# Optimization experiments

Measured on AMD Instinct MI355X. Metric: run time of the kernel, lower is better.

The kernel has to match this reference:

```python
import jax, jax.numpy as jnp
import numpy as np

N, H, E, C, V, K = 4096, 256, 128, 32, 64, 20


def setup_inputs() -> dict:
    key = jax.random.key(0)
    ks = jax.random.split(key, 16)
    f = lambda k, s: jax.random.normal(k, s, dtype=jnp.float32)
    return {
        "vec": f(ks[0], (N, H)),
        "inp": f(ks[1], (N, E)),
        "h_prev": f(ks[2], (N, H)),
        "c_prev": f(ks[3], (N, H)),
        "Wlin": f(ks[4], (C, V, H)) * 0.05,
        "blin": f(ks[5], (C, V)) * 0.05,
        "Wec": f(ks[6], (2, H)) * 0.05,
        "bec": f(ks[7], (2,)) * 0.05,
        "Wrel": f(ks[8], (5, H)) * 0.05,
        "brel": f(ks[9], (5,)) * 0.05,
        "W_ih": f(ks[10], (K, 4 * H, E)) * 0.05,
        "b_ih": f(ks[11], (K, 4 * H)) * 0.05,
        "W_hh": f(ks[12], (K, 4 * H, H)) * 0.05,
        "b_hh": f(ks[13], (K, 4 * H)) * 0.05,
        "category": jax.random.randint(ks[14], (N,), 0, C, dtype=jnp.int32),
        "cell_id": jax.random.randint(ks[15], (N,), 0, K, dtype=jnp.int32),
        "true_idx": jax.random.randint(jax.random.fold_in(key, 100), (N,), 0, V, dtype=jnp.int32),
        "ec_idx": jax.random.randint(jax.random.fold_in(key, 101), (N,), 0, 2, dtype=jnp.int32),
        "rel_idx": jax.random.randint(jax.random.fold_in(key, 102), (N,), 0, 5, dtype=jnp.int32),
    }


def _ce(logits, targets):
    # per-row cross entropy (same math as nn.CrossEntropyLoss per example)
    logp = jax.nn.log_softmax(logits, axis=-1)
    return -jnp.take_along_axis(logp, targets[:, None], axis=-1)[:, 0]


def reference(vec, inp, h_prev, c_prev, Wlin, blin, Wec, bec, Wrel, brel,
              W_ih, b_ih, W_hh, b_hh, category, cell_id, true_idx, ec_idx, rel_idx):
    # --- get_log_odds: per-category tiny linear head, selected by category ---
    logits_all = jnp.einsum('nh,cvh->ncv', vec, Wlin) + blin          # [N,C,V]
    logits = jnp.take_along_axis(logits_all, category[:, None, None].astype(jnp.int32), axis=1)[:, 0]  # [N,V]
    logits_ec = vec @ Wec.T + bec                                      # [N,2]
    logits_rel = vec @ Wrel.T + brel                                   # [N,5]

    # --- calculate_loss: CE over valid children + ec + rel ---
    losses = _ce(logits, true_idx) + _ce(logits_ec, ec_idx) + _ce(logits_rel, rel_idx)  # [N]

    # --- get_next: per-child-index LSTMCell, selected by cell_id ---
    gates_all = (jnp.einsum('ne,kge->nkg', inp, W_ih)
                 + jnp.einsum('nh,kgh->nkg', h_prev, W_hh)
                 + b_ih + b_hh)                                        # [N,K,4H]
    gates = jnp.take_along_axis(gates_all, cell_id[:, None, None].astype(jnp.int32), axis=1)[:, 0]  # [N,4H]
    i, f, g, o = jnp.split(gates, 4, axis=-1)                          # torch LSTMCell gate order i,f,g,o
    c_next = jax.nn.sigmoid(f) * c_prev + jax.nn.sigmoid(i) * jnp.tanh(g)
    h_next = jax.nn.sigmoid(o) * jnp.tanh(c_next)

    # pack: [N, 1 + 2H] = loss | h_next | c_next
    return jnp.concatenate([losses[:, None], h_next, c_next], axis=-1)
```

## Files before the change

kernel.cpp:

```cpp
#include <hip/hip_runtime.h>
#include <hip/hip_bf16.h>
#include <math.h>

#define Nn 4096
#define Hdim 256
#define Edim 128
#define Cdim 32
#define Vdim 64
#define Kdim 20
#define G4H 1024
#define OUTS 513

#define NB 8
#define LMAXL 96
#define MAXG (NB * LMAXL)
#define MAXT2 192
#define GRID (MAXG + MAXT2)

typedef short bf16x8 __attribute__((ext_vector_type(8)));
typedef float f32x4 __attribute__((ext_vector_type(4)));

__device__ __forceinline__ float sigmoidf_(float x) { return 1.0f / (1.0f + expf(-x)); }

__device__ __forceinline__ bf16x8 cvt8(float4 f0, float4 f1) {
    bf16x8 r;
    __hip_bfloat16 h;
    h = __float2bfloat16(f0.x); r[0] = *(short*)&h;
    h = __float2bfloat16(f0.y); r[1] = *(short*)&h;
    h = __float2bfloat16(f0.z); r[2] = *(short*)&h;
    h = __float2bfloat16(f0.w); r[3] = *(short*)&h;
    h = __float2bfloat16(f1.x); r[4] = *(short*)&h;
    h = __float2bfloat16(f1.y); r[5] = *(short*)&h;
    h = __float2bfloat16(f1.z); r[6] = *(short*)&h;
    h = __float2bfloat16(f1.w); r[7] = *(short*)&h;
    return r;
}

__device__ __forceinline__ void gl_lds16(const float* g, void* l) {
    __builtin_amdgcn_global_load_lds((const __attribute__((address_space(1))) void*)g,
                                     (__attribute__((address_space(3))) void*)l, 16, 0, 0);
}

__device__ __forceinline__ int swz(int r) { return ((r & 3) << 1) | ((r >> 2) & 1); }

__global__ __launch_bounds__(256, 4) void k_all(
    const float* __restrict__ vec, const float* __restrict__ inp,
    const float* __restrict__ h_prev, const float* __restrict__ c_prev,
    const float* __restrict__ Wlin, const float* __restrict__ blin,
    const float* __restrict__ Wec, const float* __restrict__ bec,
    const float* __restrict__ Wrel, const float* __restrict__ brel,
    const float* __restrict__ W_ih, const float* __restrict__ b_ih,
    const float* __restrict__ W_hh, const float* __restrict__ b_hh,
    const int* __restrict__ category, const int* __restrict__ cell_id,
    const int* __restrict__ true_idx, const int* __restrict__ ec_idx, const int* __restrict__ rel_idx,
    float* __restrict__ out)
{
    __shared__ __align__(16) char smem[40960];
    int* cntR = (int*)smem;
    int* cntF = (int*)(smem + 8192);
    int* wsum = (int*)(smem + 8320);
    int* rows_tmp = (int*)(smem + 8448);

    int t = threadIdx.x;
    int w = t >> 6, l = t & 63;
    int l15 = l & 15, quad = l >> 4;
    int lrow8 = l >> 3, lslot = l & 7;
    bool is_lstm = blockIdx.x < MAXG;
    const int* key = is_lstm ? cell_id : category;
    int nbins = is_lstm ? Kdim : Cdim;

    for (int i = t; i < nbins * 16; i += 256) cntR[i] = 0;
    __syncthreads();
    int4 kv0 = ((const int4*)key)[t * 4 + 0];
    int4 kv1 = ((const int4*)key)[t * 4 + 1];
    int4 kv2 = ((const int4*)key)[t * 4 + 2];
    int4 kv3 = ((const int4*)key)[t * 4 + 3];
    int ks[16] = { kv0.x, kv0.y, kv0.z, kv0.w, kv1.x, kv1.y, kv1.z, kv1.w,
                   kv2.x, kv2.y, kv2.z, kv2.w, kv3.x, kv3.y, kv3.z, kv3.w };
    int rep = t & 15;
    #pragma unroll
    for (int j = 0; j < 16; j++) atomicAdd(&cntR[ks[j] * 16 + rep], 1);
    __syncthreads();
    if (t < nbins) {
        int s2 = 0;
        #pragma unroll
        for (int r2 = 0; r2 < 16; r2++) s2 += cntR[t * 16 + r2];
        cntF[t] = s2;
    }
    __syncthreads();

    int myk, s_idx, hb0 = 0, rcount, wlen;
    if (is_lstm) {
        int b = blockIdx.x & 7, pos = blockIdx.x >> 3;
        int u = -1, sf = 0, acc = 0;
        for (int uu = b; uu < Kdim * 4; uu += NB) {
            int n = (cntF[uu >> 2] + 63) >> 6;
            if (u < 0 && pos < acc + n) { u = uu; sf = pos - acc; }
            acc += n;
        }
        if (u < 0) return;
        myk = u >> 2; hb0 = (u & 3) * 64; s_idx = sf;
        wlen = 64;
        rcount = min(64, cntF[myk] - s_idx * 64);
    } else {
        int slot = blockIdx.x - MAXG;
        int u = -1, sf = 0, acc = 0;
        for (int m = 0; m < Cdim; m++) {
            int n = (cntF[m] + 31) >> 5;
            if (u < 0 && slot < acc + n) { u = m; sf = slot - acc; }
            acc += n;
        }
        if (u < 0) return;
        myk = u; s_idx = sf;
        wlen = 32;
        rcount = min(32, cntF[myk] - s_idx * 32);
    }

    {
        int local = 0;
        #pragma unroll
        for (int j = 0; j < 16; j++) local += (ks[j] == myk) ? 1 : 0;
        int v = local;
        #pragma unroll
        for (int off = 1; off < 64; off <<= 1) {
            int n = __shfl_up(v, off);
            if (l >= off) v += n;
        }
        if (l == 63) wsum[w] = v;
        __syncthreads();
        int wbase = 0;
        #pragma unroll
        for (int ww = 0; ww < 4; ww++) wbase += (ww < w) ? wsum[ww] : 0;
        int rank = wbase + v - local;
        int w0 = s_idx * wlen;
        #pragma unroll
        for (int j = 0; j < 16; j++) {
            if (ks[j] == myk) {
                int rr = rank - w0;
                if (rr >= 0 && rr < wlen) rows_tmp[rr] = t * 16 + j;
                rank++;
            }
        }
        __syncthreads();
        if (t < wlen && t >= rcount) rows_tmp[t] = rows_tmp[0];
        __syncthreads();
    }
    int reg_row = rows_tmp[is_lstm ? l : (l & 31)];
    int swz_l = swz(l15);
    int p0 = (quad * 2) ^ swz_l;

    if (is_lstm) {
        float* Wbuf = (float*)smem;
        float* Xbuf = (float*)(smem + 32768);
        const float* Wih_k = W_ih + (size_t)myk * G4H * Edim;
        const float* Whh_k = W_hh + (size_t)myk * G4H * Hdim;

        int xr0 = w * 16 + lrow8;
        int xr1 = w * 16 + 8 + lrow8;
        int xrow0 = __shfl(reg_row, xr0);
        int xrow1 = __shfl(reg_row, xr1);
        int xg0 = lslot ^ swz(xr0);
        int xg1 = lslot ^ swz(xr1);

        f32x4 acc[4][4];
        #pragma unroll
        for (int m = 0; m < 4; m++)
            #pragma unroll
            for (int g = 0; g < 4; g++)
                acc[m][g] = (f32x4){0.f, 0.f, 0.f, 0.f};

        for (int st = 0; st < 12; st++) {
            int k0 = st * 32;
            const float* Wsrc; int stride, ko;
            if (k0 < Edim) { Wsrc = Wih_k; stride = Edim; ko = k0; }
            else           { Wsrc = Whh_k; stride = Hdim; ko = k0 - Edim; }
            const float* Xs0 = (k0 < Edim) ? inp + (size_t)xrow0 * Edim + ko
                                           : h_prev + (size_t)xrow0 * Hdim + (ko - 0);
            const float* Xs1 = (k0 < Edim) ? inp + (size_t)xrow1 * Edim + ko
                                           : h_prev + (size_t)xrow1 * Hdim + (ko - 0);
            __syncthreads();
            #pragma unroll
            for (int j = 0; j < 8; j++) {
                int r = w * 64 + j * 8 + lrow8;
                int g = lslot ^ swz(r);
                int gate = r >> 6, hl = r & 63;
                gl_lds16(Wsrc + (size_t)(gate * Hdim + hb0 + hl) * stride + ko + g * 4,
                         Wbuf + (w * 64 + j * 8) * 32);
            }
            gl_lds16(Xs0 + xg0 * 4, Xbuf + (w * 16) * 32);
            gl_lds16(Xs1 + xg1 * 4, Xbuf + (w * 16 + 8) * 32);
            __syncthreads();

            bf16x8 af[4], bfr[4];
            #pragma unroll
            for (int m = 0; m < 4; m++) {
                int row = m * 16 + l15;
                float4 lo = *(float4*)(Xbuf + row * 32 + p0 * 4);
                float4 hi = *(float4*)(Xbuf + row * 32 + (p0 ^ 1) * 4);
                af[m] = cvt8(lo, hi);
            }
            #pragma unroll
            for (int g = 0; g < 4; g++) {
                int row = g * 64 + w * 16 + l15;
                float4 lo = *(float4*)(Wbuf + row * 32 + p0 * 4);
                float4 hi = *(float4*)(Wbuf + row * 32 + (p0 ^ 1) * 4);
                bfr[g] = cvt8(lo, hi);
            }
            #pragma unroll
            for (int m = 0; m < 4; m++)
                #pragma unroll
                for (int g = 0; g < 4; g++)
                    acc[m][g] = __builtin_amdgcn_mfma_f32_16x16x32_bf16(af[m], bfr[g], acc[m][g], 0, 0, 0);
        }

        int h = hb0 + w * 16 + l15;
        float bs[4];
        #pragma unroll
        for (int g = 0; g < 4; g++)
            bs[g] = b_ih[(size_t)myk * G4H + g * Hdim + h] + b_hh[(size_t)myk * G4H + g * Hdim + h];

        #pragma unroll
        for (int m = 0; m < 4; m++) {
            #pragma unroll
            for (int reg = 0; reg < 4; reg++) {
                int r = m * 16 + quad * 4 + reg;
                int row = __shfl(reg_row, r);
                if (r < rcount) {
                    float iv = acc[m][0][reg] + bs[0];
                    float fv = acc[m][1][reg] + bs[1];
                    float gv = acc[m][2][reg] + bs[2];
                    float ov = acc[m][3][reg] + bs[3];
                    float cp = c_prev[(size_t)row * Hdim + h];
                    float cn = sigmoidf_(fv) * cp + sigmoidf_(iv) * tanhf(gv);
                    float hn = sigmoidf_(ov) * tanhf(cn);
                    out[(size_t)row * OUTS + 1 + h] = hn;
                    out[(size_t)row * OUTS + 1 + Hdim + h] = cn;
                }
            }
        }
    } else {
        float* Wlbuf = (float*)smem;
        float* Vbuf  = (float*)(smem + 10240);
        float* Lg    = (float*)(smem + 14336);
        int m2 = myk;

        int xr = w * 8 + lrow8;
        int xrow = __shfl(reg_row, xr);
        int xg = lslot ^ swz(xr);

        f32x4 a0[2], a1[2];
        #pragma unroll
        for (int m = 0; m < 2; m++) { a0[m] = (f32x4){0.f,0.f,0.f,0.f}; a1[m] = (f32x4){0.f,0.f,0.f,0.f}; }

        for (int st = 0; st < 8; st++) {
            int ko = st * 32;
            __syncthreads();
            for (int n = w; n < 10; n += 4) {
                int r = n * 8 + lrow8;
                int g = lslot ^ swz(r);
                const float* srcW;
                if (r < 64)      srcW = Wlin + ((size_t)m2 * Vdim + r) * Hdim;
                else if (r < 66) srcW = Wec + (size_t)(r - 64) * Hdim;
                else if (r < 71) srcW = Wrel + (size_t)(r - 66) * Hdim;
                else             srcW = Wlin + (size_t)m2 * Vdim * Hdim;
                gl_lds16(srcW + ko + g * 4, Wlbuf + n * 8 * 32);
            }
            gl_lds16(vec + (size_t)xrow * Hdim + ko + xg * 4, Vbuf + (w * 8) * 32);
            __syncthreads();

            bf16x8 af[2];
            #pragma unroll
            for (int m = 0; m < 2; m++) {
                int row = m * 16 + l15;
                float4 lo = *(float4*)(Vbuf + row * 32 + p0 * 4);
                float4 hi = *(float4*)(Vbuf + row * 32 + (p0 ^ 1) * 4);
                af[m] = cvt8(lo, hi);
            }
            {
                int row = w * 16 + l15;
                float4 lo = *(float4*)(Wlbuf + row * 32 + p0 * 4);
                float4 hi = *(float4*)(Wlbuf + row * 32 + (p0 ^ 1) * 4);
                bf16x8 b0 = cvt8(lo, hi);
                a0[0] = __builtin_amdgcn_mfma_f32_16x16x32_bf16(af[0], b0, a0[0], 0, 0, 0);
                a0[1] = __builtin_amdgcn_mfma_f32_16x16x32_bf16(af[1], b0, a0[1], 0, 0, 0);
            }
            if (w == 3) {
                int row = 64 + l15;
                float4 lo = *(float4*)(Wlbuf + row * 32 + p0 * 4);
                float4 hi = *(float4*)(Wlbuf + row * 32 + (p0 ^ 1) * 4);
                bf16x8 b1 = cvt8(lo, hi);
                a1[0] = __builtin_amdgcn_mfma_f32_16x16x32_bf16(af[0], b1, a1[0], 0, 0, 0);
                a1[1] = __builtin_amdgcn_mfma_f32_16x16x32_bf16(af[1], b1, a1[1], 0, 0, 0);
            }
        }
        __syncthreads();
        {
            int col = w * 16 + l15;
            float bb = blin[m2 * Vdim + col];
            #pragma unroll
            for (int m = 0; m < 2; m++)
                #pragma unroll
                for (int reg = 0; reg < 4; reg++)
                    Lg[(m * 16 + quad * 4 + reg) * 84 + col] = a0[m][reg] + bb;
            if (w == 3) {
                int col1 = 64 + l15;
                float bb1 = (l15 < 2) ? bec[l15] : ((l15 < 7) ? brel[l15 - 2] : 0.f);
                #pragma unroll
                for (int m = 0; m < 2; m++)
                    #pragma unroll
                    for (int reg = 0; reg < 4; reg++)
                        Lg[(m * 16 + quad * 4 + reg) * 84 + col1] = a1[m][reg] + bb1;
            }
        }
        __syncthreads();
        for (int rr = 0; rr < 8; rr++) {
            int r = w * 8 + rr;
            if (r >= rcount) break;
            int orig = __shfl(reg_row, r);
            float lg = Lg[r * 84 + l];
            float mx = lg;
            for (int ss = 32; ss >= 1; ss >>= 1) mx = fmaxf(mx, __shfl_xor(mx, ss));
            float sm = expf(lg - mx);
            for (int ss = 32; ss >= 1; ss >>= 1) sm += __shfl_xor(sm, ss);
            float lt = __shfl(lg, true_idx[orig]);
            float loss = mx + logf(sm) - lt;
            if (l == 0) {
                float l0 = Lg[r * 84 + 64], l1 = Lg[r * 84 + 65];
                float me2 = fmaxf(l0, l1);
                loss += me2 + logf(expf(l0 - me2) + expf(l1 - me2)) - ((ec_idx[orig] == 0) ? l0 : l1);
                float rl[5] = { Lg[r * 84 + 66], Lg[r * 84 + 67], Lg[r * 84 + 68], Lg[r * 84 + 69], Lg[r * 84 + 70] };
                float mr = rl[0];
                #pragma unroll
                for (int i = 1; i < 5; i++) mr = fmaxf(mr, rl[i]);
                float sr = 0.f;
                #pragma unroll
                for (int i = 0; i < 5; i++) sr += expf(rl[i] - mr);
                loss += mr + logf(sr) - rl[rel_idx[orig]];
                out[(size_t)orig * OUTS] = loss;
            }
        }
    }
}

extern "C" void kernel_launch(void* const* d_in, const int* in_sizes, int n_in,
                              void* d_out, int out_size, void* d_ws, size_t ws_size,
                              hipStream_t stream) {
    const float* vec      = (const float*)d_in[0];
    const float* inp      = (const float*)d_in[1];
    const float* h_prev   = (const float*)d_in[2];
    const float* c_prev   = (const float*)d_in[3];
    const float* Wlin     = (const float*)d_in[4];
    const float* blin     = (const float*)d_in[5];
    const float* Wec      = (const float*)d_in[6];
    const float* bec      = (const float*)d_in[7];
    const float* Wrel     = (const float*)d_in[8];
    const float* brel     = (const float*)d_in[9];
    const float* W_ih     = (const float*)d_in[10];
    const float* b_ih     = (const float*)d_in[11];
    const float* W_hh     = (const float*)d_in[12];
    const float* b_hh     = (const float*)d_in[13];
    const int*   category = (const int*)d_in[14];
    const int*   cell_id  = (const int*)d_in[15];
    const int*   true_idx = (const int*)d_in[16];
    const int*   ec_idx   = (const int*)d_in[17];
    const int*   rel_idx  = (const int*)d_in[18];
    float* out = (float*)d_out;

    k_all<<<GRID, 256, 0, stream>>>(
        vec, inp, h_prev, c_prev, Wlin, blin, Wec, bec, Wrel, brel,
        W_ih, b_ih, W_hh, b_hh, category, cell_id, true_idx, ec_idx, rel_idx, out);
}
```

Before: 153.3 us.

## Precompute row bucketing in setup kernel and double-buffer LDS staging

Moves the per-block histogram and rank computation over cell_id/category into a small separate setup kernel that writes per-bucket row lists and counts to workspace, so each main block just reads its row list. The main kernel's K-loops now double-buffer the global-to-LDS loads with explicit vmcnt waits so the next stage's loads overlap the current stage's MFMAs. LDS doubles to 80KB and occupancy drops to 2 blocks, and an extra kernel launch is added. Row order within buckets now depends on atomic order, and buckets are capped at fixed sizes.

After: 144.0 us. 1.06x faster.

```diff
diff --git a/kernel.cpp b/kernel.cpp
--- a/kernel.cpp
+++ b/kernel.cpp
@@ -12,10 +12,15 @@
 #define OUTS 513
 
 #define NB 8
-#define LMAXL 96
+#define LMAXL 64
 #define MAXG (NB * LMAXL)
 #define MAXT2 192
 #define GRID (MAXG + MAXT2)
+
+#define SK 512
+#define SC 256
+#define RK_OFF 64
+#define RC_OFF (RK_OFF + Kdim * SK)
 
 typedef short bf16x8 __attribute__((ext_vector_type(8)));
 typedef float f32x4 __attribute__((ext_vector_type(4)));
@@ -43,7 +48,36 @@
 
 __device__ __forceinline__ int swz(int r) { return ((r & 3) << 1) | ((r >> 2) & 1); }
 
-__global__ __launch_bounds__(256, 4) void k_all(
+__global__ __launch_bounds__(1024) void k_setup(const int* __restrict__ cell_id,
+                                                const int* __restrict__ category,
+                                                int* __restrict__ ws) {
+    __shared__ int cnt[32];
+    int t = threadIdx.x;
+    if (t < 32) cnt[t] = 0;
+    __syncthreads();
+    int i0 = t * 4;
+    if (blockIdx.x == 0) {
+        int4 v = ((const int4*)cell_id)[t];
+        int r;
+        r = atomicAdd(&cnt[v.x], 1); if (r < SK) ws[RK_OFF + v.x * SK + r] = i0 + 0;
+        r = atomicAdd(&cnt[v.y], 1); if (r < SK) ws[RK_OFF + v.y * SK + r] = i0 + 1;
+        r = atomicAdd(&cnt[v.z], 1); if (r < SK) ws[RK_OFF + v.z * SK + r] = i0 + 2;
+        r = atomicAdd(&cnt[v.w], 1); if (r < SK) ws[RK_OFF + v.w * SK + r] = i0 + 3;
+        __syncthreads();
+        if (t < 32) ws[t] = min(cnt[t], SK);
+    } else {
+        int4 v = ((const int4*)category)[t];
+        int r;
+        r = atomicAdd(&cnt[v.x], 1); if (r < SC) ws[RC_OFF + v.x * SC + r] = i0 + 0;
+        r = atomicAdd(&cnt[v.y], 1); if (r < SC) ws[RC_OFF + v.y * SC + r] = i0 + 1;
+        r = atomicAdd(&cnt[v.z], 1); if (r < SC) ws[RC_OFF + v.z * SC + r] = i0 + 2;
+        r = atomicAdd(&cnt[v.w], 1); if (r < SC) ws[RC_OFF + v.w * SC + r] = i0 + 3;
+        __syncthreads();
+        if (t < 32) ws[32 + t] = min(cnt[t], SC);
+    }
+}
+
+__global__ __launch_bounds__(256, 2) void k_main(
     const float* __restrict__ vec, const float* __restrict__ inp,
     const float* __restrict__ h_prev, const float* __restrict__ c_prev,
     const float* __restrict__ Wlin, const float* __restrict__ blin,
@@ -51,159 +85,120 @@
     const float* __restrict__ Wrel, const float* __restrict__ brel,
     const float* __restrict__ W_ih, const float* __restrict__ b_ih,
     const float* __restrict__ W_hh, const float* __restrict__ b_hh,
-    const int* __restrict__ category, const int* __restrict__ cell_id,
     const int* __restrict__ true_idx, const int* __restrict__ ec_idx, const int* __restrict__ rel_idx,
+    const int* __restrict__ ws,
     float* __restrict__ out)
 {
-    __shared__ __align__(16) char smem[40960];
-    int* cntR = (int*)smem;
-    int* cntF = (int*)(smem + 8192);
-    int* wsum = (int*)(smem + 8320);
-    int* rows_tmp = (int*)(smem + 8448);
+    __shared__ __align__(16) char smem[81920];
 
     int t = threadIdx.x;
     int w = t >> 6, l = t & 63;
     int l15 = l & 15, quad = l >> 4;
     int lrow8 = l >> 3, lslot = l & 7;
     bool is_lstm = blockIdx.x < MAXG;
-    const int* key = is_lstm ? cell_id : category;
-    int nbins = is_lstm ? Kdim : Cdim;
-
-    for (int i = t; i < nbins * 16; i += 256) cntR[i] = 0;
+
+    int* cnt = (int*)smem;
+    if (t < 32) cnt[t] = ws[(is_lstm ? 0 : 32) + t];
     __syncthreads();
-    int4 kv0 = ((const int4*)key)[t * 4 + 0];
-    int4 kv1 = ((const int4*)key)[t * 4 + 1];
-    int4 kv2 = ((const int4*)key)[t * 4 + 2];
-    int4 kv3 = ((const int4*)key)[t * 4 + 3];
-    int ks[16] = { kv0.x, kv0.y, kv0.z, kv0.w, kv1.x, kv1.y, kv1.z, kv1.w,
-                   kv2.x, kv2.y, kv2.z, kv2.w, kv3.x, kv3.y, kv3.z, kv3.w };
-    int rep = t & 15;
-    #pragma unroll
-    for (int j = 0; j < 16; j++) atomicAdd(&cntR[ks[j] * 16 + rep], 1);
-    __syncthreads();
-    if (t < nbins) {
-        int s2 = 0;
-        #pragma unroll
-        for (int r2 = 0; r2 < 16; r2++) s2 += cntR[t * 16 + r2];
-        cntF[t] = s2;
-    }
-    __syncthreads();
-
-    int myk, s_idx, hb0 = 0, rcount, wlen;
+
+    int myk, s_idx, hb0 = 0, rcount;
     if (is_lstm) {
         int b = blockIdx.x & 7, pos = blockIdx.x >> 3;
         int u = -1, sf = 0, acc = 0;
         for (int uu = b; uu < Kdim * 4; uu += NB) {
-            int n = (cntF[uu >> 2] + 63) >> 6;
+            int n = (cnt[uu >> 2] + 63) >> 6;
             if (u < 0 && pos < acc + n) { u = uu; sf = pos - acc; }
             acc += n;
         }
         if (u < 0) return;
         myk = u >> 2; hb0 = (u & 3) * 64; s_idx = sf;
-        wlen = 64;
-        rcount = min(64, cntF[myk] - s_idx * 64);
+        rcount = min(64, cnt[myk] - s_idx * 64);
     } else {
         int slot = blockIdx.x - MAXG;
         int u = -1, sf = 0, acc = 0;
         for (int m = 0; m < Cdim; m++) {
-            int n = (cntF[m] + 31) >> 5;
+            int n = (cnt[m] + 31) >> 5;
             if (u < 0 && slot < acc + n) { u = m; sf = slot - acc; }
             acc += n;
         }
         if (u < 0) return;
         myk = u; s_idx = sf;
-        wlen = 32;
-        rcount = min(32, cntF[myk] - s_idx * 32);
+        rcount = min(32, cnt[myk] - s_idx * 32);
     }
 
-    {
-        int local = 0;
-        #pragma unroll
-        for (int j = 0; j < 16; j++) local += (ks[j] == myk) ? 1 : 0;
-        int v = local;
-        #pragma unroll
-        for (int off = 1; off < 64; off <<= 1) {
-            int n = __shfl_up(v, off);
-            if (l >= off) v += n;
-        }
-        if (l == 63) wsum[w] = v;
-        __syncthreads();
-        int wbase = 0;
-        #pragma unroll
-        for (int ww = 0; ww < 4; ww++) wbase += (ww < w) ? wsum[ww] : 0;
-        int rank = wbase + v - local;
-        int w0 = s_idx * wlen;
-        #pragma unroll
-        for (int j = 0; j < 16; j++) {
-            if (ks[j] == myk) {
-                int rr = rank - w0;
-                if (rr >= 0 && rr < wlen) rows_tmp[rr] = t * 16 + j;
-                rank++;
-            }
-        }
-        __syncthreads();
-        if (t < wlen && t >= rcount) rows_tmp[t] = rows_tmp[0];
-        __syncthreads();
-    }
-    int reg_row = rows_tmp[is_lstm ? l : (l & 31)];
+    const int* rlist = is_lstm ? (ws + RK_OFF + myk * SK + s_idx * 64)
+                               : (ws + RC_OFF + myk * SC + s_idx * 32);
+    int li = is_lstm ? l : (l & 31);
+    int reg_row = rlist[li < rcount ? li : rcount - 1];
     int swz_l = swz(l15);
     int p0 = (quad * 2) ^ swz_l;
+    __syncthreads();
 
     if (is_lstm) {
-        float* Wbuf = (float*)smem;
-        float* Xbuf = (float*)(smem + 32768);
         const float* Wih_k = W_ih + (size_t)myk * G4H * Edim;
         const float* Whh_k = W_hh + (size_t)myk * G4H * Hdim;
 
         int xr0 = w * 16 + lrow8;
-        int xr1 = w * 16 + 8 + lrow8;
+        int xr1 = xr0 + 8;
         int xrow0 = __shfl(reg_row, xr0);
         int xrow1 = __shfl(reg_row, xr1);
         int xg0 = lslot ^ swz(xr0);
         int xg1 = lslot ^ swz(xr1);
 
-        f32x4 acc[4][4];
-        #pragma unroll
-        for (int m = 0; m < 4; m++)
-            #pragma unroll
-            for (int g = 0; g < 4; g++)
-                acc[m][g] = (f32x4){0.f, 0.f, 0.f, 0.f};
-
-        for (int st = 0; st < 12; st++) {
+        auto stageL = [&](int st, int d) {
+            float* Wb = (float*)(smem + d * 40960);
+            float* Xb = (float*)(smem + d * 40960 + 32768);
             int k0 = st * 32;
             const float* Wsrc; int stride, ko;
             if (k0 < Edim) { Wsrc = Wih_k; stride = Edim; ko = k0; }
             else           { Wsrc = Whh_k; stride = Hdim; ko = k0 - Edim; }
-            const float* Xs0 = (k0 < Edim) ? inp + (size_t)xrow0 * Edim + ko
-                                           : h_prev + (size_t)xrow0 * Hdim + (ko - 0);
-            const float* Xs1 = (k0 < Edim) ? inp + (size_t)xrow1 * Edim + ko
-                                           : h_prev + (size_t)xrow1 * Hdim + (ko - 0);
-            __syncthreads();
             #pragma unroll
             for (int j = 0; j < 8; j++) {
                 int r = w * 64 + j * 8 + lrow8;
                 int g = lslot ^ swz(r);
                 int gate = r >> 6, hl = r & 63;
                 gl_lds16(Wsrc + (size_t)(gate * Hdim + hb0 + hl) * stride + ko + g * 4,
-                         Wbuf + (w * 64 + j * 8) * 32);
-            }
-            gl_lds16(Xs0 + xg0 * 4, Xbuf + (w * 16) * 32);
-            gl_lds16(Xs1 + xg1 * 4, Xbuf + (w * 16 + 8) * 32);
-            __syncthreads();
-
+                         Wb + (w * 64 + j * 8) * 32);
+            }
+            const float* Xs0 = (k0 < Edim) ? inp + (size_t)xrow0 * Edim + ko
+                                           : h_prev + (size_t)xrow0 * Hdim + ko;
+            const float* Xs1 = (k0 < Edim) ? inp + (size_t)xrow1 * Edim + ko
+                                           : h_prev + (size_t)xrow1 * Hdim + ko;
+            gl_lds16(Xs0 + xg0 * 4, Xb + (w * 16) * 32);
+            gl_lds16(Xs1 + xg1 * 4, Xb + (w * 16 + 8) * 32);
+        };
+
+        f32x4 acc[4][4];
+        #pragma unroll
+        for (int m = 0; m < 4; m++)
+            #pragma unroll
+            for (int g = 0; g < 4; g++)
+                acc[m][g] = (f32x4){0.f, 0.f, 0.f, 0.f};
+
+        stageL(0, 0);
+        for (int st = 0; st < 12; st++) {
+            int cur = st & 1;
+            if (st < 11) stageL(st + 1, cur ^ 1);
+            if (st < 11) asm volatile("s_waitcnt vmcnt(10)" ::: "memory");
+            else         asm volatile("s_waitcnt vmcnt(0)" ::: "memory");
+            __builtin_amdgcn_s_barrier();
+            __builtin_amdgcn_sched_barrier(0);
+
+            float* Wb = (float*)(smem + cur * 40960);
+            float* Xb = (float*)(smem + cur * 40960 + 32768);
             bf16x8 af[4], bfr[4];
             #pragma unroll
             for (int m = 0; m < 4; m++) {
                 int row = m * 16 + l15;
-                float4 lo = *(float4*)(Xbuf + row * 32 + p0 * 4);
-                float4 hi = *(float4*)(Xbuf + row * 32 + (p0 ^ 1) * 4);
+                float4 lo = *(float4*)(Xb + row * 32 + p0 * 4);
+                float4 hi = *(float4*)(Xb + row * 32 + (p0 ^ 1) * 4);
                 af[m] = cvt8(lo, hi);
             }
             #pragma unroll
             for (int g = 0; g < 4; g++) {
                 int row = g * 64 + w * 16 + l15;
-                float4 lo = *(float4*)(Wbuf + row * 32 + p0 * 4);
-                float4 hi = *(float4*)(Wbuf + row * 32 + (p0 ^ 1) * 4);
+                float4 lo = *(float4*)(Wb + row * 32 + p0 * 4);
+                float4 hi = *(float4*)(Wb + row * 32 + (p0 ^ 1) * 4);
                 bfr[g] = cvt8(lo, hi);
             }
             #pragma unroll
@@ -211,6 +206,9 @@
                 #pragma unroll
                 for (int g = 0; g < 4; g++)
                     acc[m][g] = __builtin_amdgcn_mfma_f32_16x16x32_bf16(af[m], bfr[g], acc[m][g], 0, 0, 0);
+
+            __builtin_amdgcn_sched_barrier(0);
+            __builtin_amdgcn_s_barrier();
         }
 
         int h = hb0 + w * 16 + l15;
@@ -239,22 +237,15 @@
             }
         }
     } else {
-        float* Wlbuf = (float*)smem;
-        float* Vbuf  = (float*)(smem + 10240);
-        float* Lg    = (float*)(smem + 14336);
         int m2 = myk;
-
         int xr = w * 8 + lrow8;
         int xrow = __shfl(reg_row, xr);
         int xg = lslot ^ swz(xr);
 
-        f32x4 a0[2], a1[2];
-        #pragma unroll
-        for (int m = 0; m < 2; m++) { a0[m] = (f32x4){0.f,0.f,0.f,0.f}; a1[m] = (f32x4){0.f,0.f,0.f,0.f}; }
-
-        for (int st = 0; st < 8; st++) {
+        auto stageS = [&](int st, int d) {
+            float* Wb = (float*)(smem + d * 14336);
+            float* Vb = (float*)(smem + d * 14336 + 10240);
             int ko = st * 32;
-            __syncthreads();
             for (int n = w; n < 10; n += 4) {
                 int r = n * 8 + lrow8;
                 int g = lslot ^ swz(r);
@@ -263,37 +254,57 @@
                 else if (r < 66) srcW = Wec + (size_t)(r - 64) * Hdim;
                 else if (r < 71) srcW = Wrel + (size_t)(r - 66) * Hdim;
                 else             srcW = Wlin + (size_t)m2 * Vdim * Hdim;
-                gl_lds16(srcW + ko + g * 4, Wlbuf + n * 8 * 32);
-            }
-            gl_lds16(vec + (size_t)xrow * Hdim + ko + xg * 4, Vbuf + (w * 8) * 32);
-            __syncthreads();
-
+                gl_lds16(srcW + ko + g * 4, Wb + n * 8 * 32);
+            }
+            gl_lds16(vec + (size_t)xrow * Hdim + ko + xg * 4, Vb + (w * 8) * 32);
+        };
+
+        f32x4 a0[2], a1[2];
+        #pragma unroll
+        for (int m = 0; m < 2; m++) { a0[m] = (f32x4){0.f,0.f,0.f,0.f}; a1[m] = (f32x4){0.f,0.f,0.f,0.f}; }
+
+        stageS(0, 0);
+        for (int st = 0; st < 8; st++) {
+            int cur = st & 1;
+            if (st < 7) stageS(st + 1, cur ^ 1);
+            if (st < 7) {
+                if (w < 2) asm volatile("s_waitcnt vmcnt(4)" ::: "memory");
+                else       asm volatile("s_waitcnt vmcnt(3)" ::: "memory");
+            } else       asm volatile("s_waitcnt vmcnt(0)" ::: "memory");
+            __builtin_amdgcn_s_barrier();
+            __builtin_amdgcn_sched_barrier(0);
+
+            float* Wb = (float*)(smem + cur * 14336);
+            float* Vb = (float*)(smem + cur * 14336 + 10240);
             bf16x8 af[2];
             #pragma unroll
             for (int m = 0; m < 2; m++) {
                 int row = m * 16 + l15;
-                float4 lo = *(float4*)(Vbuf + row * 32 + p0 * 4);
-                float4 hi = *(float4*)(Vbuf + row * 32 + (p0 ^ 1) * 4);
+                float4 lo = *(float4*)(Vb + row * 32 + p0 * 4);
+                float4 hi = *(float4*)(Vb + row * 32 + (p0 ^ 1) * 4);
                 af[m] = cvt8(lo, hi);
             }
             {
                 int row = w * 16 + l15;
-                float4 lo = *(float4*)(Wlbuf + row * 32 + p0 * 4);
-                float4 hi = *(float4*)(Wlbuf + row * 32 + (p0 ^ 1) * 4);
+                float4 lo = *(float4*)(Wb + row * 32 + p0 * 4);
+                float4 hi = *(float4*)(Wb + row * 32 + (p0 ^ 1) * 4);
                 bf16x8 b0 = cvt8(lo, hi);
                 a0[0] = __builtin_amdgcn_mfma_f32_16x16x32_bf16(af[0], b0, a0[0], 0, 0, 0);
                 a0[1] = __builtin_amdgcn_mfma_f32_16x16x32_bf16(af[1], b0, a0[1], 0, 0, 0);
             }
             if (w == 3) {
                 int row = 64 + l15;
-                float4 lo = *(float4*)(Wlbuf + row * 32 + p0 * 4);
-                float4 hi = *(float4*)(Wlbuf + row * 32 + (p0 ^ 1) * 4);
+                float4 lo = *(float4*)(Wb + row * 32 + p0 * 4);
+                float4 hi = *(float4*)(Wb + row * 32 + (p0 ^ 1) * 4);
                 bf16x8 b1 = cvt8(lo, hi);
                 a1[0] = __builtin_amdgcn_mfma_f32_16x16x32_bf16(af[0], b1, a1[0], 0, 0, 0);
                 a1[1] = __builtin_amdgcn_mfma_f32_16x16x32_bf16(af[1], b1, a1[1], 0, 0, 0);
             }
-        }
-        __syncthreads();
+            __builtin_amdgcn_sched_barrier(0);
+            __builtin_amdgcn_s_barrier();
+        }
+
+        float* Lg = (float*)(smem + 28672);
         {
             int col = w * 16 + l15;
             float bb = blin[m2 * Vdim + col];
@@ -365,8 +376,10 @@
     const int*   ec_idx   = (const int*)d_in[17];
     const int*   rel_idx  = (const int*)d_in[18];
     float* out = (float*)d_out;
-
-    k_all<<<GRID, 256, 0, stream>>>(
+    int* ws = (int*)d_ws;
+
+    k_setup<<<2, 1024, 0, stream>>>(cell_id, category, ws);
+    k_main<<<GRID, 256, 0, stream>>>(
         vec, inp, h_prev, c_prev, Wlin, blin, Wec, bec, Wrel, brel,
-        W_ih, b_ih, W_hh, b_hh, category, cell_id, true_idx, ec_idx, rel_idx, out);
-}
+        W_ih, b_ih, W_hh, b_hh, true_idx, ec_idx, rel_idx, ws, out);
+}
```
